# Performance work log

Measured on AMD Instinct MI355X. Metric: run time of the kernel, lower is better.

## Reference

```python
import jax, jax.numpy as jnp
import numpy as np

B, N, F_IN, F_OUT = 8, 8192, 128, 128
E = 1_048_576
BN = B * N


def setup_inputs() -> dict:
    key = jax.random.key(0)
    ks = jax.random.split(key, 9)
    glorot = (6.0 / (F_IN + F_OUT)) ** 0.5
    return {
        "X": jax.random.normal(ks[0], (B, N, F_IN), dtype=jnp.float32),
        "W0": jax.random.uniform(ks[1], (F_IN, F_OUT), jnp.float32, -glorot, glorot),
        "W1": jax.random.uniform(ks[2], (F_IN, F_OUT), jnp.float32, -glorot, glorot),
        "rows0": jax.random.randint(ks[3], (E,), 0, BN, dtype=jnp.int32),
        "cols0": jax.random.randint(ks[4], (E,), 0, BN, dtype=jnp.int32),
        "vals0": jax.random.uniform(ks[5], (E,), dtype=jnp.float32),
        "rows1": jax.random.randint(ks[6], (E,), 0, BN, dtype=jnp.int32),
        "cols1": jax.random.randint(ks[7], (E,), 0, BN, dtype=jnp.int32),
        "vals1": jax.random.uniform(ks[8], (E,), dtype=jnp.float32),
    }


def _spmm(rows, cols, vals, H, n):
    # COO sparse [n, n] @ dense H [n, F]: gather source rows, scale, scatter-add.
    return jax.ops.segment_sum(vals[:, None] * H[cols], rows, num_segments=n)


def reference(X, W0, W1, rows0, cols0, vals0, rows1, cols1, vals1):
    b, n, f_in = X.shape
    X2 = X.reshape(-1, f_in)                      # [B*N, F_in]
    h0 = _spmm(rows0, cols0, vals0, X2 @ W0, b * n)  # filter_0 @ (X W0)
    h1 = _spmm(rows1, cols1, vals1, X2 @ W1, b * n)  # filter_1 @ (X W1)
    out = jax.nn.relu(h0 + h1).reshape(b, n, -1)  # add_n + relu
    return out
```

## Files before the change

kernel.cpp:

```cpp
#include <hip/hip_runtime.h>


typedef unsigned int   uint;
typedef unsigned short ushort;
typedef unsigned char  uchar;
typedef float f32x4 __attribute__((ext_vector_type(4)));
typedef int   i32x4 __attribute__((ext_vector_type(4)));

constexpr int NBK  = 512;
constexpr int RPB  = 128;
constexpr int EPB  = 8192;
constexpr int GCAP = 3584;
constexpr int CAP  = 3072;

__device__ __forceinline__ ushort f2bf(float f) {
    uint u = __float_as_uint(f);
    u += 0x7fffu + ((u >> 16) & 1u);
    return (ushort)(u >> 16);
}
__device__ __forceinline__ float bf2f(ushort h) {
    return __uint_as_float((uint)h << 16);
}

#define ACC_FENCE(a) asm volatile("s_nop 7\n\ts_nop 7" : "+v"(a))

__global__ __launch_bounds__(64) void w_swz(const float* __restrict__ W0,
                                            const float* __restrict__ W1,
                                            uint4* __restrict__ Wswz,
                                            int* __restrict__ cur_g) {
    const int bx = blockIdx.x;
    const int l  = threadIdx.x;
    if (bx == 64) {
        for (int i = l; i < 2 * NBK; i += 64) cur_g[i] = 0;
        return;
    }
    const int f  = bx >> 5;
    const int ct = (bx >> 2) & 7;
    const int kt = bx & 3;
    const float* W = f ? W1 : W0;
    const int kbase = kt * 32 + (l >> 4) * 8;
    const int col   = ct * 16 + (l & 15);
    ushort h[8];
#pragma unroll
    for (int j = 0; j < 8; ++j)
        h[j] = f2bf(W[(kbase + j) * 128 + col]);
    uint4 o;
    o.x = (uint)h[0] | ((uint)h[1] << 16);
    o.y = (uint)h[2] | ((uint)h[3] << 16);
    o.z = (uint)h[4] | ((uint)h[5] << 16);
    o.w = (uint)h[6] | ((uint)h[7] << 16);
    Wswz[((f * 8 + ct) * 4 + kt) * 64 + l] = o;
}

__global__ __launch_bounds__(256) void gemm_mfma(const float* __restrict__ X,
                                                 const i32x4* __restrict__ Wswz,
                                                 ushort* __restrict__ H, int BN) {
    __shared__ ushort xs_hi[64][136];
    __shared__ ushort xs_lo[64][136];
    const int tid = threadIdx.x;
    const int l = tid & 63;
    const int w = tid >> 6;
    const long rbase = (long)blockIdx.x * 64;

    const float4* Xv = reinterpret_cast<const float4*>(X + rbase * 128);
#pragma unroll
    for (int i = 0; i < 8; ++i) {
        int idx = i * 256 + tid;
        int row = idx >> 5, c4 = idx & 31;
        float4 v = Xv[idx];
        ushort4 hi, lo;
        hi.x = f2bf(v.x); lo.x = f2bf(v.x - bf2f(hi.x));
        hi.y = f2bf(v.y); lo.y = f2bf(v.y - bf2f(hi.y));
        hi.z = f2bf(v.z); lo.z = f2bf(v.z - bf2f(hi.z));
        hi.w = f2bf(v.w); lo.w = f2bf(v.w - bf2f(hi.w));
        *reinterpret_cast<ushort4*>(&xs_hi[row][c4 * 4]) = hi;
        *reinterpret_cast<ushort4*>(&xs_lo[row][c4 * 4]) = lo;
    }
    __syncthreads();

    i32x4 a_hi[4], a_lo[4];
    const int arow = w * 16 + (l & 15);
    const int kb = (l >> 4) * 8;
#pragma unroll
    for (int kt = 0; kt < 4; ++kt) {
        a_hi[kt] = *reinterpret_cast<const i32x4*>(&xs_hi[arow][kt * 32 + kb]);
        a_lo[kt] = *reinterpret_cast<const i32x4*>(&xs_lo[arow][kt * 32 + kb]);
    }

    f32x4 acc[2][8];
#pragma unroll
    for (int f = 0; f < 2; ++f)
#pragma unroll
        for (int ct = 0; ct < 8; ++ct)
            acc[f][ct] = (f32x4)0.0f;

#pragma unroll
    for (int ct = 0; ct < 8; ++ct)
#pragma unroll
        for (int f = 0; f < 2; ++f)
#pragma unroll
            for (int kt = 0; kt < 4; ++kt) {
                i32x4 b = Wswz[((f * 8 + ct) * 4 + kt) * 64 + l];
                asm volatile("v_mfma_f32_16x16x32_bf16 %0, %1, %2, %0"
                             : "+v"(acc[f][ct]) : "v"(a_hi[kt]), "v"(b));
                asm volatile("v_mfma_f32_16x16x32_bf16 %0, %1, %2, %0"
                             : "+v"(acc[f][ct]) : "v"(a_lo[kt]), "v"(b));
            }

#pragma unroll
    for (int ct = 0; ct < 8; ++ct)
#pragma unroll
        for (int f = 0; f < 2; ++f) {
            f32x4 a = acc[f][ct];
            ACC_FENCE(a);
            ushort* Hf = H + (size_t)f * BN * 128;
            size_t base = (size_t)(rbase + w * 16 + (l >> 4) * 4) * 128
                        + ct * 16 + (l & 15);
            Hf[base]       = f2bf(a.x);
            Hf[base + 128] = f2bf(a.y);
            Hf[base + 256] = f2bf(a.z);
            Hf[base + 384] = f2bf(a.w);
        }
}

__global__ __launch_bounds__(1024) void partition(const int* __restrict__ r0,
                                                  const int* __restrict__ c0,
                                                  const float* __restrict__ v0,
                                                  const int* __restrict__ r1,
                                                  const int* __restrict__ c1,
                                                  const float* __restrict__ v1,
                                                  int* __restrict__ cur_g,
                                                  uint* __restrict__ cvy,
                                                  uchar* __restrict__ cvr, int E) {
    __shared__ int h[NBK];
    __shared__ int cur[NBK];
    const int f = blockIdx.y, t = threadIdx.x;
    const int*   rows = f ? r1 : r0;
    const int*   cols = f ? c1 : c0;
    const float* vals = f ? v1 : v0;
    const int base = blockIdx.x * EPB;

    if (t < NBK) h[t] = 0;
    __syncthreads();
#pragma unroll
    for (int k = 0; k < EPB / 1024; ++k) {
        int e = base + k * 1024 + t;
        if (e < E) atomicAdd(&h[rows[e] >> 7], 1);
    }
    __syncthreads();
    if (t < NBK)
        cur[t] = atomicAdd(&cur_g[f * NBK + t], h[t]);
    __syncthreads();

#pragma unroll
    for (int k = 0; k < EPB / 1024; ++k) {
        int e = base + k * 1024 + t;
        if (e < E) {
            int r = rows[e];
            int b = r >> 7;
            int pos = atomicAdd(&cur[b], 1);
            if (pos < GCAP) {
                size_t idx = (size_t)(f * NBK + b) * GCAP + pos;
                cvy[idx] = ((uint)cols[e] << 16) | (uint)f2bf(vals[e]);
                cvr[idx] = (uchar)(r & 127);
            }
        }
    }
}

__device__ __forceinline__ void fma4(float4& a, float v, ushort4 h) {
    a.x = fmaf(v, bf2f(h.x), a.x);
    a.y = fmaf(v, bf2f(h.y), a.y);
    a.z = fmaf(v, bf2f(h.z), a.z);
    a.w = fmaf(v, bf2f(h.w), a.w);
}

__global__ __launch_bounds__(512) void sort_gather(
        const uint* __restrict__ cvy, const uchar* __restrict__ cvr,
        const int* __restrict__ cur_g,
        const ushort* __restrict__ H, int BN,
        float* __restrict__ out) {
    __shared__ uint cvl[2][CAP];
    __shared__ int rp[2][RPB + 1];
    __shared__ int hcnt[RPB];
    __shared__ int curs[RPB];
    __shared__ int scount[2], sovf[2];

    const int b = blockIdx.x;
    const int t = threadIdx.x;

#pragma unroll 1
    for (int f = 0; f < 2; ++f) {
        if (t == 0) {
            int n0 = cur_g[f * NBK + b];
            if (n0 > GCAP) n0 = GCAP;
            scount[f] = n0;
            sovf[f]   = n0 > CAP;
        }
        if (t < RPB) hcnt[t] = 0;
        __syncthreads();
        const int n = scount[f];
        const uchar* rin = cvr + (size_t)(f * NBK + b) * GCAP;
        const uint*  yin = cvy + (size_t)(f * NBK + b) * GCAP;
        for (int i = t; i < n; i += 512)
            atomicAdd(&hcnt[rin[i]], 1);
        __syncthreads();
        int v = (t < RPB) ? hcnt[t] : 0;
        if (t < RPB) curs[t] = v;
        __syncthreads();
        for (int off = 1; off < RPB; off <<= 1) {
            int u = 0;
            if (t < RPB && t >= off) u = curs[t - off];
            __syncthreads();
            if (t < RPB) curs[t] += u;
            __syncthreads();
        }
        if (t < RPB) {
            int ex = curs[t] - v;
            rp[f][t] = ex;
            curs[t] = ex;
        }
        if (t == 0) rp[f][RPB] = n;
        __syncthreads();
        if (!sovf[f]) {
            for (int i = t; i < n; i += 512) {
                uchar r = rin[i];
                int pos = atomicAdd(&curs[r], 1);
                cvl[f][pos] = __builtin_nontemporal_load(&yin[i]);
            }
        }
        __syncthreads();
    }

    const int half = t >> 5;
    const int sub  = t & 31;
    f32x4* outv = reinterpret_cast<f32x4*>(out);

#pragma unroll 1
    for (int k = 0; k < 8; ++k) {
        const int lr = k * 16 + half;
        const long gr = (long)b * RPB + lr;

        float4 a0 = make_float4(0.f, 0.f, 0.f, 0.f);
        float4 a1 = make_float4(0.f, 0.f, 0.f, 0.f);
        float4 a2 = make_float4(0.f, 0.f, 0.f, 0.f);
        float4 a3 = make_float4(0.f, 0.f, 0.f, 0.f);

#pragma unroll
        for (int f = 0; f < 2; ++f) {
            const ushort* Hf = H + (size_t)f * BN * 128;
            if (!sovf[f]) {
                int e = rp[f][lr];
                const int e1 = rp[f][lr + 1];
                for (; e + 7 < e1; e += 8) {
                    uint p0 = cvl[f][e],     p1 = cvl[f][e + 1];
                    uint p2 = cvl[f][e + 2], p3 = cvl[f][e + 3];
                    uint p4 = cvl[f][e + 4], p5 = cvl[f][e + 5];
                    uint p6 = cvl[f][e + 6], p7 = cvl[f][e + 7];
                    ushort4 h0 = reinterpret_cast<const ushort4*>(Hf + (size_t)(p0 >> 16) * 128)[sub];
                    ushort4 h1 = reinterpret_cast<const ushort4*>(Hf + (size_t)(p1 >> 16) * 128)[sub];
                    ushort4 h2 = reinterpret_cast<const ushort4*>(Hf + (size_t)(p2 >> 16) * 128)[sub];
                    ushort4 h3 = reinterpret_cast<const ushort4*>(Hf + (size_t)(p3 >> 16) * 128)[sub];
                    ushort4 h4 = reinterpret_cast<const ushort4*>(Hf + (size_t)(p4 >> 16) * 128)[sub];
                    ushort4 h5 = reinterpret_cast<const ushort4*>(Hf + (size_t)(p5 >> 16) * 128)[sub];
                    ushort4 h6 = reinterpret_cast<const ushort4*>(Hf + (size_t)(p6 >> 16) * 128)[sub];
                    ushort4 h7 = reinterpret_cast<const ushort4*>(Hf + (size_t)(p7 >> 16) * 128)[sub];
                    fma4(a0, __uint_as_float(p0 << 16), h0);
                    fma4(a1, __uint_as_float(p1 << 16), h1);
                    fma4(a2, __uint_as_float(p2 << 16), h2);
                    fma4(a3, __uint_as_float(p3 << 16), h3);
                    fma4(a0, __uint_as_float(p4 << 16), h4);
                    fma4(a1, __uint_as_float(p5 << 16), h5);
                    fma4(a2, __uint_as_float(p6 << 16), h6);
                    fma4(a3, __uint_as_float(p7 << 16), h7);
                }
                for (; e + 3 < e1; e += 4) {
                    uint p0 = cvl[f][e],     p1 = cvl[f][e + 1];
                    uint p2 = cvl[f][e + 2], p3 = cvl[f][e + 3];
                    ushort4 h0 = reinterpret_cast<const ushort4*>(Hf + (size_t)(p0 >> 16) * 128)[sub];
                    ushort4 h1 = reinterpret_cast<const ushort4*>(Hf + (size_t)(p1 >> 16) * 128)[sub];
                    ushort4 h2 = reinterpret_cast<const ushort4*>(Hf + (size_t)(p2 >> 16) * 128)[sub];
                    ushort4 h3 = reinterpret_cast<const ushort4*>(Hf + (size_t)(p3 >> 16) * 128)[sub];
                    fma4(a0, __uint_as_float(p0 << 16), h0);
                    fma4(a1, __uint_as_float(p1 << 16), h1);
                    fma4(a2, __uint_as_float(p2 << 16), h2);
                    fma4(a3, __uint_as_float(p3 << 16), h3);
                }
                for (; e < e1; ++e) {
                    uint p0 = cvl[f][e];
                    ushort4 h0 = reinterpret_cast<const ushort4*>(Hf + (size_t)(p0 >> 16) * 128)[sub];
                    fma4(a0, __uint_as_float(p0 << 16), h0);
                }
            } else {
                const int n = scount[f];
                const uchar* rin = cvr + (size_t)(f * NBK + b) * GCAP;
                const uint*  yin = cvy + (size_t)(f * NBK + b) * GCAP;
                for (int i = 0; i < n; ++i) {
                    if (rin[i] == (uchar)lr) {
                        uint p0 = yin[i];
                        ushort4 h0 = reinterpret_cast<const ushort4*>(Hf + (size_t)(p0 >> 16) * 128)[sub];
                        fma4(a0, __uint_as_float(p0 << 16), h0);
                    }
                }
            }
        }

        f32x4 o;
        o.x = fmaxf((a0.x + a1.x) + (a2.x + a3.x), 0.0f);
        o.y = fmaxf((a0.y + a1.y) + (a2.y + a3.y), 0.0f);
        o.z = fmaxf((a0.z + a1.z) + (a2.z + a3.z), 0.0f);
        o.w = fmaxf((a0.w + a1.w) + (a2.w + a3.w), 0.0f);
        __builtin_nontemporal_store(o, outv + gr * 32 + sub);
    }
}

extern "C" void kernel_launch(void* const* d_in, const int* in_sizes, int n_in,
                              void* d_out, int out_size, void* d_ws, size_t ws_size,
                              hipStream_t stream) {
    const float* X     = (const float*)d_in[0];
    const float* W0    = (const float*)d_in[1];
    const float* W1    = (const float*)d_in[2];
    const int*   rows0 = (const int*)d_in[3];
    const int*   cols0 = (const int*)d_in[4];
    const float* vals0 = (const float*)d_in[5];
    const int*   rows1 = (const int*)d_in[6];
    const int*   cols1 = (const int*)d_in[7];
    const float* vals1 = (const float*)d_in[8];
    float* out = (float*)d_out;

    const int BN = in_sizes[0] / 128;
    const int E  = in_sizes[3];
    const int partb = (E + EPB - 1) / EPB;

    char* ws = (char*)d_ws;
    size_t off = 0;
    auto alloc = [&](size_t bytes) {
        void* p = ws + off;
        off = (off + bytes + 255) & ~(size_t)255;
        return p;
    };
    ushort* H     = (ushort*)alloc((size_t)2 * BN * 128 * sizeof(ushort));
    uint4*  Wswz  = (uint4*) alloc((size_t)2 * 128 * 128 * sizeof(ushort));
    uint*   cvy   = (uint*)  alloc((size_t)2 * NBK * GCAP * sizeof(uint));
    uchar*  cvr   = (uchar*) alloc((size_t)2 * NBK * GCAP * sizeof(uchar));
    int*    cur_g = (int*)   alloc((size_t)2 * NBK * sizeof(int));

    w_swz<<<65, 64, 0, stream>>>(W0, W1, Wswz, cur_g);
    gemm_mfma<<<BN / 64, 256, 0, stream>>>(X, (const i32x4*)Wswz, H, BN);
    partition<<<dim3(partb, 2), 1024, 0, stream>>>(rows0, cols0, vals0,
                                                   rows1, cols1, vals1,
                                                   cur_g, cvy, cvr, E);
    sort_gather<<<NBK, 512, 0, stream>>>(cvy, cvr, cur_g, H, BN, out);
}
```

Measured before the change: 147.8 us.

## Fuse GEMM and edge partition into one launch; load X fragments directly

Merges the MFMA GEMM and the COO partition kernels into a single launch whose first 2*partb blocks do the partitioning and the rest do the GEMM, so the two independent phases can run concurrently. The partition blocks shrink from 1024 to 256 threads with non-unrolled loops. The GEMM also drops its LDS staging and builds the bf16 hi/lo A fragments straight from global memory, removing a barrier and the shared buffers at the cost of less coalesced X loads.

```diff
diff --git a/kernel.cpp b/kernel.cpp
--- a/kernel.cpp
+++ b/kernel.cpp
@@ -52,39 +52,90 @@
     Wswz[((f * 8 + ct) * 4 + kt) * 64 + l] = o;
 }
 
-__global__ __launch_bounds__(256) void gemm_mfma(const float* __restrict__ X,
-                                                 const i32x4* __restrict__ Wswz,
-                                                 ushort* __restrict__ H, int BN) {
-    __shared__ ushort xs_hi[64][136];
-    __shared__ ushort xs_lo[64][136];
-    const int tid = threadIdx.x;
-    const int l = tid & 63;
-    const int w = tid >> 6;
-    const long rbase = (long)blockIdx.x * 64;
-
-    const float4* Xv = reinterpret_cast<const float4*>(X + rbase * 128);
-#pragma unroll
-    for (int i = 0; i < 8; ++i) {
-        int idx = i * 256 + tid;
-        int row = idx >> 5, c4 = idx & 31;
-        float4 v = Xv[idx];
-        ushort4 hi, lo;
-        hi.x = f2bf(v.x); lo.x = f2bf(v.x - bf2f(hi.x));
-        hi.y = f2bf(v.y); lo.y = f2bf(v.y - bf2f(hi.y));
-        hi.z = f2bf(v.z); lo.z = f2bf(v.z - bf2f(hi.z));
-        hi.w = f2bf(v.w); lo.w = f2bf(v.w - bf2f(hi.w));
-        *reinterpret_cast<ushort4*>(&xs_hi[row][c4 * 4]) = hi;
-        *reinterpret_cast<ushort4*>(&xs_lo[row][c4 * 4]) = lo;
-    }
-    __syncthreads();
-
-    i32x4 a_hi[4], a_lo[4];
+__device__ __forceinline__ uint pack2bf(float a, float b) {
+    return (uint)f2bf(a) | ((uint)f2bf(b) << 16);
+}
+
+__global__ __launch_bounds__(256) void gemm_part(
+        const float* __restrict__ X, const i32x4* __restrict__ Wswz,
+        ushort* __restrict__ H, int BN,
+        const int* __restrict__ r0, const int* __restrict__ c0,
+        const float* __restrict__ v0,
+        const int* __restrict__ r1, const int* __restrict__ c1,
+        const float* __restrict__ v1,
+        int* __restrict__ cur_g, uint* __restrict__ cvy,
+        uchar* __restrict__ cvr, int E, int partb) {
+    __shared__ int h[NBK];
+    __shared__ int cur[NBK];
+    const int bx = blockIdx.x;
+    const int t  = threadIdx.x;
+
+    if (bx < 2 * partb) {
+        const int f  = bx / partb;
+        const int px = bx % partb;
+        const int*   rows = f ? r1 : r0;
+        const int*   cols = f ? c1 : c0;
+        const float* vals = f ? v1 : v0;
+        const int base = px * EPB;
+
+        h[t] = 0; h[t + 256] = 0;
+        __syncthreads();
+#pragma unroll 1
+        for (int k = 0; k < EPB / 256; ++k) {
+            int e = base + k * 256 + t;
+            if (e < E) atomicAdd(&h[rows[e] >> 7], 1);
+        }
+        __syncthreads();
+        cur[t]       = atomicAdd(&cur_g[f * NBK + t],       h[t]);
+        cur[t + 256] = atomicAdd(&cur_g[f * NBK + t + 256], h[t + 256]);
+        __syncthreads();
+
+#pragma unroll 1
+        for (int k = 0; k < EPB / 256; ++k) {
+            int e = base + k * 256 + t;
+            if (e < E) {
+                int r = rows[e];
+                int b = r >> 7;
+                int pos = atomicAdd(&cur[b], 1);
+                if (pos < GCAP) {
+                    size_t idx = (size_t)(f * NBK + b) * GCAP + pos;
+                    cvy[idx] = ((uint)cols[e] << 16) | (uint)f2bf(vals[e]);
+                    cvr[idx] = (uchar)(r & 127);
+                }
+            }
+        }
+        return;
+    }
+
+    const int gx = bx - 2 * partb;
+    const int l = t & 63;
+    const int w = t >> 6;
+    const long rbase = (long)gx * 64;
     const int arow = w * 16 + (l & 15);
     const int kb = (l >> 4) * 8;
+
+    const float* Xr = X + (rbase + arow) * 128;
+    i32x4 a_hi[4], a_lo[4];
 #pragma unroll
     for (int kt = 0; kt < 4; ++kt) {
-        a_hi[kt] = *reinterpret_cast<const i32x4*>(&xs_hi[arow][kt * 32 + kb]);
-        a_lo[kt] = *reinterpret_cast<const i32x4*>(&xs_lo[arow][kt * 32 + kb]);
+        float4 u0 = *reinterpret_cast<const float4*>(Xr + kt * 32 + kb);
+        float4 u1 = *reinterpret_cast<const float4*>(Xr + kt * 32 + kb + 4);
+        float e0, e1;
+        i32x4 hi, lo;
+        hi.x = (int)pack2bf(u0.x, u0.y);
+        e0 = u0.x - bf2f(f2bf(u0.x)); e1 = u0.y - bf2f(f2bf(u0.y));
+        lo.x = (int)pack2bf(e0, e1);
+        hi.y = (int)pack2bf(u0.z, u0.w);
+        e0 = u0.z - bf2f(f2bf(u0.z)); e1 = u0.w - bf2f(f2bf(u0.w));
+        lo.y = (int)pack2bf(e0, e1);
+        hi.z = (int)pack2bf(u1.x, u1.y);
+        e0 = u1.x - bf2f(f2bf(u1.x)); e1 = u1.y - bf2f(f2bf(u1.y));
+        lo.z = (int)pack2bf(e0, e1);
+        hi.w = (int)pack2bf(u1.z, u1.w);
+        e0 = u1.z - bf2f(f2bf(u1.z)); e1 = u1.w - bf2f(f2bf(u1.w));
+        lo.w = (int)pack2bf(e0, e1);
+        a_hi[kt] = hi;
+        a_lo[kt] = lo;
     }
 
     f32x4 acc[2][8];
@@ -121,51 +172,6 @@
             Hf[base + 256] = f2bf(a.z);
             Hf[base + 384] = f2bf(a.w);
         }
-}
-
-__global__ __launch_bounds__(1024) void partition(const int* __restrict__ r0,
-                                                  const int* __restrict__ c0,
-                                                  const float* __restrict__ v0,
-                                                  const int* __restrict__ r1,
-                                                  const int* __restrict__ c1,
-                                                  const float* __restrict__ v1,
-                                                  int* __restrict__ cur_g,
-                                                  uint* __restrict__ cvy,
-                                                  uchar* __restrict__ cvr, int E) {
-    __shared__ int h[NBK];
-    __shared__ int cur[NBK];
-    const int f = blockIdx.y, t = threadIdx.x;
-    const int*   rows = f ? r1 : r0;
-    const int*   cols = f ? c1 : c0;
-    const float* vals = f ? v1 : v0;
-    const int base = blockIdx.x * EPB;
-
-    if (t < NBK) h[t] = 0;
-    __syncthreads();
-#pragma unroll
-    for (int k = 0; k < EPB / 1024; ++k) {
-        int e = base + k * 1024 + t;
-        if (e < E) atomicAdd(&h[rows[e] >> 7], 1);
-    }
-    __syncthreads();
-    if (t < NBK)
-        cur[t] = atomicAdd(&cur_g[f * NBK + t], h[t]);
-    __syncthreads();
-
-#pragma unroll
-    for (int k = 0; k < EPB / 1024; ++k) {
-        int e = base + k * 1024 + t;
-        if (e < E) {
-            int r = rows[e];
-            int b = r >> 7;
-            int pos = atomicAdd(&cur[b], 1);
-            if (pos < GCAP) {
-                size_t idx = (size_t)(f * NBK + b) * GCAP + pos;
-                cvy[idx] = ((uint)cols[e] << 16) | (uint)f2bf(vals[e]);
-                cvr[idx] = (uchar)(r & 127);
-            }
-        }
-    }
 }
 
 __device__ __forceinline__ void fma4(float4& a, float v, ushort4 h) {
@@ -346,9 +352,9 @@
     int*    cur_g = (int*)   alloc((size_t)2 * NBK * sizeof(int));
 
     w_swz<<<65, 64, 0, stream>>>(W0, W1, Wswz, cur_g);
-    gemm_mfma<<<BN / 64, 256, 0, stream>>>(X, (const i32x4*)Wswz, H, BN);
-    partition<<<dim3(partb, 2), 1024, 0, stream>>>(rows0, cols0, vals0,
-                                                   rows1, cols1, vals1,
-                                                   cur_g, cvy, cvr, E);
+    gemm_part<<<2 * partb + BN / 64, 256, 0, stream>>>(
+        X, (const i32x4*)Wswz, H, BN,
+        rows0, cols0, vals0, rows1, cols1, vals1,
+        cur_g, cvy, cvr, E, partb);
     sort_gather<<<NBK, 512, 0, stream>>>(cvy, cvr, cur_g, H, BN, out);
 }
```

Measured after the change: 144.7 us (median of 2 runs). 2.1% less time.
